# Kernel tuning notes

Measured on AMD Instinct MI355X. Metric: run time of the kernel, lower is better.

## Reference

```python
import jax, jax.numpy as jnp
import numpy as np

TAU = 0.6      # init_tau (membrane decay, also scales surrogate h_t)
TAU_O = 0.6    # init_tau_o (output / eligibility kappa filter)
THR = 0.6      # init_thresh (spike threshold)
LR = 0.05      # e-prop grad accumulation factor


def setup_inputs() -> dict:
    key = jax.random.key(0)
    k0, k1, k2, k3, k4 = jax.random.split(key, 5)
    B, T, NI, NH, NO = 64, 100, 700, 512, 20
    # binary spike inputs / one-hot-ish labels (rand -> threshold keeps SNN semantics)
    x = (jax.random.uniform(k0, (B, T, NI)) < 0.3).astype(jnp.float32)
    label = (jax.random.uniform(k1, (B, T, NO)) < 0.5).astype(jnp.float32)
    # kaiming_normal_ then *0.5 for fc1/out; kaiming_normal_ for recurrent
    w_fc1 = jax.random.normal(k2, (NH, NI), jnp.float32) * (0.5 * np.sqrt(2.0 / NI))
    w_rec = jax.random.normal(k3, (NH, NH), jnp.float32) * np.sqrt(2.0 / NH)
    w_out = jax.random.normal(k4, (NO, NH), jnp.float32) * (0.5 * np.sqrt(2.0 / NH))
    return dict(x=x, label=label, training=1, w_fc1=w_fc1, w_rec=w_rec, w_out=w_out)


def reference(x, label, training, w_fc1, w_rec, w_out):
    B, T, NI = x.shape
    NH = w_fc1.shape[0]
    NO = w_out.shape[0]
    dt = x.dtype

    def step(carry, xs):
        (hm, hs, om, os, tin, trec, tout, ein, erec, prev_hs, gf, gr, go) = carry
        xt, lt = xs  # [B,NI], [B,NO]
        # LIF hidden: decay (with reset-by-spike) + input + recurrent
        hidden_input = xt @ w_fc1.T + hs @ w_rec
        hm = TAU * hm * (1.0 - hs) + hidden_input
        hs = (hm >= THR).astype(dt)
        # LIF output
        om = TAU * om * (1.0 - os) + hs @ w_out.T
        os = (om >= THR).astype(dt)
        err = os - lt
        # surrogate derivative (triangle)
        h_t = TAU * jnp.maximum(0.0, 1.0 - jnp.abs((hm - THR) / THR))
        # presynaptic traces (trace_rec uses z_{t-1})
        tin = TAU * tin + xt
        trec = TAU * trec + prev_hs
        # eligibility traces: per-sample outer products, kappa-filtered
        ein = TAU_O * ein + h_t[:, :, None] * tin[:, None, :]    # [B,NH,NI]
        erec = TAU_O * erec + h_t[:, :, None] * trec[:, None, :]  # [B,NH,NH]
        tout = TAU_O * tout + hs
        # learning signal broadcast from output error
        L = err @ w_out  # [B,NH]
        gf = gf + LR * jnp.einsum('br,bri->ri', L, ein)
        gr = gr + LR * jnp.einsum('br,brj->rj', L, erec)
        go = go + LR * jnp.einsum('bo,br->or', err, tout)
        return (hm, hs, om, os, tin, trec, tout, ein, erec, hs, gf, gr, go), os

    z = lambda *s: jnp.zeros(s, dt)
    carry0 = (z(B, NH), z(B, NH), z(B, NO), z(B, NO), z(B, NI), z(B, NH),
              z(B, NH), z(B, NH, NI), z(B, NH, NH), z(B, NH),
              z(NH, NI), z(NH, NH), z(NO, NH))
    xs = (jnp.swapaxes(x, 0, 1), jnp.swapaxes(label, 0, 1))  # time-major
    carryF, outs = jax.lax.scan(step, carry0, xs)
    outputs = jnp.swapaxes(outs, 0, 1)  # [B,T,NO]
    return outputs, carryF[10], carryF[11], carryF[12]
```

## Files before the change

kernel.cpp:

```cpp
#include <hip/hip_runtime.h>
#include <hip/hip_bf16.h>

constexpr int kB  = 64;
constexpr int kT  = 100;
constexpr int kNI = 700;
constexpr int kNH = 512;
constexpr int kNO = 20;
constexpr float TAU   = 0.6f;
constexpr float TAU_O = 0.6f;
constexpr float THR   = 0.6f;
constexpr float LR    = 0.05f;

constexpr size_t BNH = (size_t)kB * kNH;
constexpr size_t BNI = (size_t)kB * kNI;
constexpr size_t BNO = (size_t)kB * kNO;
constexpr int kK   = kT * kB;
constexpr int kKP  = 704;

typedef __attribute__((ext_vector_type(8))) short short8;
typedef __attribute__((ext_vector_type(4))) float f32x4;

constexpr size_t O_XW   = 0;
constexpr size_t O_PGF  = 0;
constexpr size_t O_PGR  = 1572864;
constexpr size_t O_PGO  = 2621440;
constexpr size_t O_HSUR = 3276800;
constexpr size_t O_ERR  = 6553600;
constexpr size_t O_MTB  = 6681600;
constexpr size_t O_TRB  = 8320000;
constexpr size_t O_MSK  = 9958400;
constexpr size_t O_TIB  = 10060800;
constexpr size_t WS_FLOATS = 12300800;

constexpr size_t OUT_GF = (size_t)kB * kT * kNO;
constexpr size_t OUT_GR = OUT_GF + (size_t)kNH * kNI;
constexpr size_t OUT_GO = OUT_GR + (size_t)kNH * kNH;

__global__ __launch_bounds__(256) void k_xw2(const float* __restrict__ x,
                                             const float* __restrict__ wfc,
                                             float* __restrict__ XW) {
    int bx = blockIdx.x;
    int mt = bx % 50, nt = bx / 50;
    int m0 = mt * 128, n0 = nt * 128;
    int tid = threadIdx.x, tx = tid & 15, ty = tid >> 4;
    __shared__ float As[128][20];
    __shared__ float Bs[16][128];
    float acc[8][8] = {};
    int arow = tid >> 1, ahalf = tid & 1;
    int bb = (m0 + arow) & 63, tt = (m0 + arow) >> 6;
    const float* ap = x + ((size_t)bb * kT + tt) * kNI;
    const float* wp = wfc + (size_t)(n0 + arow) * kNI;
    for (int k0 = 0; k0 < kKP; k0 += 16) {
        #pragma unroll
        for (int u = 0; u < 2; u++) {
            int k = k0 + ahalf * 8 + u * 4;
            float4 v = (k + 3 < kNI) ? *(const float4*)(ap + k)
                                     : make_float4(0.f, 0.f, 0.f, 0.f);
            *(float4*)&As[arow][ahalf * 8 + u * 4] = v;
        }
        {
            int kb = k0 + ahalf * 8;
            float4 v0 = (kb + 3 < kNI) ? *(const float4*)(wp + kb)
                                       : make_float4(0.f, 0.f, 0.f, 0.f);
            float4 v1 = (kb + 7 < kNI) ? *(const float4*)(wp + kb + 4)
                                       : make_float4(0.f, 0.f, 0.f, 0.f);
            int c = ahalf * 8;
            Bs[c + 0][arow] = v0.x; Bs[c + 1][arow] = v0.y;
            Bs[c + 2][arow] = v0.z; Bs[c + 3][arow] = v0.w;
            Bs[c + 4][arow] = v1.x; Bs[c + 5][arow] = v1.y;
            Bs[c + 6][arow] = v1.z; Bs[c + 7][arow] = v1.w;
        }
        __syncthreads();
        #pragma unroll
        for (int kk = 0; kk < 16; kk++) {
            float av[8];
            #pragma unroll
            for (int i = 0; i < 4; i++) {
                av[i]     = As[ty * 4 + i][kk];
                av[4 + i] = As[64 + ty * 4 + i][kk];
            }
            float4 b0 = *(const float4*)&Bs[kk][tx * 4];
            float4 b1 = *(const float4*)&Bs[kk][64 + tx * 4];
            float bvv[8] = {b0.x, b0.y, b0.z, b0.w, b1.x, b1.y, b1.z, b1.w};
            #pragma unroll
            for (int i = 0; i < 8; i++)
                #pragma unroll
                for (int j = 0; j < 8; j++) acc[i][j] += av[i] * bvv[j];
        }
        __syncthreads();
    }
    #pragma unroll
    for (int i = 0; i < 8; i++) {
        int m = m0 + ((i < 4) ? (ty * 4 + i) : (64 + ty * 4 + i - 4));
        float* dst = XW + (size_t)m * kNH + n0;
        *(float4*)(dst + tx * 4)      = make_float4(acc[i][0], acc[i][1], acc[i][2], acc[i][3]);
        *(float4*)(dst + 64 + tx * 4) = make_float4(acc[i][4], acc[i][5], acc[i][6], acc[i][7]);
    }
}

__global__ __launch_bounds__(832) void k_forward(float* __restrict__ ws,
                                                 const float* __restrict__ label,
                                                 const float* __restrict__ w_rec,
                                                 const float* __restrict__ w_out,
                                                 float* __restrict__ dout,
                                                 unsigned long long* __restrict__ gmask,
                                                 const float* __restrict__ x) {
    __shared__ float wout_ld[kNO * kNH];
    __shared__ float partial[8][kNH];
    __shared__ unsigned long long mh[kT * 8];
    __shared__ float errh[kT * kNO];

    int bxg = blockIdx.x, tid = threadIdx.x;
    if (bxg >= kB) {
        int idx = (bxg - kB) * 832 + tid;
        if (idx < (int)BNI) {
            int b = idx / kNI, i = idx - b * kNI;
            const float* xp = x + (size_t)b * kT * kNI + i;
            unsigned short* tib = (unsigned short*)(ws + O_TIB);
            size_t rowoff = (size_t)i * kK + (size_t)b * 100;
            float v = 0.f;
            for (int tq = 0; tq < 25; tq++) {
                unsigned long long w8 = 0;
                #pragma unroll
                for (int u = 0; u < 4; u++) {
                    int t = tq * 4 + u;
                    v = TAU * v + xp[(size_t)t * kNI];
                    __hip_bfloat16 bv = __float2bfloat16(v);
                    w8 |= ((unsigned long long)*(unsigned short*)&bv) << (16 * u);
                }
                *(unsigned long long*)&tib[rowoff + tq * 4] = w8;
            }
        }
        return;
    }

    int b = bxg;
    int wave = tid >> 6, lane = tid & 63;
    const f32x4* wr4 = (const f32x4*)w_rec;
    for (int e = tid; e < kNO * kNH; e += 832) wout_ld[e] = w_out[e];
    float hm = 0.f, sp_prev = 0.f;
    float om_r[4] = {0.f, 0.f, 0.f, 0.f}, os_r[4] = {0.f, 0.f, 0.f, 0.f};
    int q = wave - 8;
    const int coff = lane * 2;
    __syncthreads();

    for (int t = 0; t < kT; t++) {
        float xw = 0.f;
        if (wave < 8) {
            xw = ws[O_XW + ((size_t)t * 64 + b) * kNH + tid];
            unsigned long long m = (t > 0) ? mh[(t - 1) * 8 + wave] : 0ull;
            const size_t base = (size_t)wave * 64;
            f32x4 s0 = {0.f, 0.f, 0.f, 0.f}, s1 = s0;
            while (m) {
                int j = __builtin_ctzll(m); m &= m - 1;
                const f32x4* r = wr4 + (base + j) * 128 + coff;
                s0 += r[0]; s1 += r[1];
            }
            *(f32x4*)&partial[wave][lane * 8]     = s0;
            *(f32x4*)&partial[wave][lane * 8 + 4] = s1;
        } else if (t > 0) {
            int to = t - 1;
            unsigned long long mk[8];
            #pragma unroll
            for (int k = 0; k < 8; k++) mk[k] = mh[to * 8 + k];
            #pragma unroll
            for (int r = 0; r < 4; r++) {
                int o = q * 4 + r;
                float p = 0.f;
                #pragma unroll
                for (int k = 0; k < 8; k++)
                    if ((mk[k] >> lane) & 1) p += wout_ld[o * kNH + 64 * k + lane];
                #pragma unroll
                for (int off = 32; off >= 1; off >>= 1) p += __shfl_xor(p, off);
                if (lane == 0) {
                    float om_n = TAU * om_r[r] * (1.f - os_r[r]) + p;
                    float os_n = (om_n >= THR) ? 1.f : 0.f;
                    om_r[r] = om_n; os_r[r] = os_n;
                    errh[to * kNO + o] = os_n - label[((size_t)b * kT + to) * kNO + o];
                    dout[((size_t)b * kT + to) * kNO + o] = os_n;
                }
            }
        }
        __syncthreads();
        if (tid < kNH) {
            float rec = ((partial[0][tid] + partial[1][tid]) + (partial[2][tid] + partial[3][tid]))
                      + ((partial[4][tid] + partial[5][tid]) + (partial[6][tid] + partial[7][tid]));
            hm = TAU * hm * (1.f - sp_prev) + (xw + rec);
            bool v = (hm >= THR);
            float sp = v ? 1.f : 0.f;
            sp_prev = sp;
            ws[O_HSUR + (size_t)t * BNH + (size_t)b * kNH + tid] =
                TAU * fmaxf(0.f, 1.f - fabsf(hm - THR) * (1.f / THR));
            unsigned long long bal = __ballot(v);
            if (lane == 0) {
                mh[t * 8 + wave] = bal;
                gmask[((size_t)t * 64 + b) * 8 + wave] = bal;
            }
        }
        __syncthreads();
    }
    if (wave >= 8) {
        int to = kT - 1;
        unsigned long long mk[8];
        #pragma unroll
        for (int k = 0; k < 8; k++) mk[k] = mh[to * 8 + k];
        #pragma unroll
        for (int r = 0; r < 4; r++) {
            int o = q * 4 + r;
            float p = 0.f;
            #pragma unroll
            for (int k = 0; k < 8; k++)
                if ((mk[k] >> lane) & 1) p += wout_ld[o * kNH + 64 * k + lane];
            #pragma unroll
            for (int off = 32; off >= 1; off >>= 1) p += __shfl_xor(p, off);
            if (lane == 0) {
                float om_n = TAU * om_r[r] * (1.f - os_r[r]) + p;
                float os_n = (om_n >= THR) ? 1.f : 0.f;
                errh[to * kNO + o] = os_n - label[((size_t)b * kT + to) * kNO + o];
                dout[((size_t)b * kT + to) * kNO + o] = os_n;
            }
        }
    }
    if (tid < kNH) {
        unsigned short* trb = (unsigned short*)(ws + O_TRB);
        size_t rowoff = (size_t)tid * kK + (size_t)b * 100;
        int w = tid >> 6, bit = tid & 63;
        float v = 0.f, p = 0.f;
        for (int tq = 0; tq < 25; tq++) {
            unsigned long long w8 = 0;
            #pragma unroll
            for (int u = 0; u < 4; u++) {
                int t = tq * 4 + u;
                v = TAU * v + p;
                __hip_bfloat16 bv = __float2bfloat16(v);
                w8 |= ((unsigned long long)*(unsigned short*)&bv) << (16 * u);
                p = (float)((mh[t * 8 + w] >> bit) & 1ull);
            }
            *(unsigned long long*)&trb[rowoff + tq * 4] = w8;
        }
    }
    __syncthreads();
    if (wave == 8 && lane < kNO) {
        float v = 0.f;
        for (int t = kT - 1; t >= 0; t--) {
            v = errh[t * kNO + lane] + TAU_O * v;
            errh[t * kNO + lane] = v;
            ws[O_ERR + (size_t)t * BNO + (size_t)b * kNO + lane] = v;
        }
    }
    __syncthreads();
    if (tid < kNH) {
        float wreg[kNO];
        #pragma unroll
        for (int o = 0; o < kNO; o++) wreg[o] = wout_ld[o * kNH + tid];
        unsigned short* mtb = (unsigned short*)(ws + O_MTB);
        size_t rowoff = (size_t)tid * kK + (size_t)b * 100;
        for (int tq = 0; tq < 25; tq++) {
            unsigned long long w8 = 0;
            #pragma unroll
            for (int u = 0; u < 4; u++) {
                int t = tq * 4 + u;
                float s = 0.f;
                #pragma unroll
                for (int o = 0; o < kNO; o++) s += errh[t * kNO + o] * wreg[o];
                float val = LR * s * ws[O_HSUR + (size_t)t * BNH + (size_t)b * kNH + tid];
                __hip_bfloat16 bv = __float2bfloat16(val);
                w8 |= ((unsigned long long)*(unsigned short*)&bv) << (16 * u);
            }
            *(unsigned long long*)&mtb[rowoff + tq * 4] = w8;
        }
    }
}

__global__ __launch_bounds__(256) void k_grads(float* __restrict__ ws) {
    __shared__ unsigned short As[128 * 72];
    __shared__ unsigned short Bs[128 * 72];
    int bx = blockIdx.x, tid = threadIdx.x;

    if (bx < 160) {
        constexpr int KC = kK / 4, BK = 64, LDT = 72;
        const unsigned short* A = (const unsigned short*)(ws + O_MTB);
        const unsigned short* B;
        float* Cpart;
        int Nrows, ldc, s, mt, nt;
        if (bx < 96) {
            s = bx & 3; mt = (bx >> 2) & 3; nt = bx >> 4;
            B = (const unsigned short*)(ws + O_TIB);
            Cpart = ws + O_PGF; Nrows = kNI; ldc = 768;
        } else {
            int v = bx - 96;
            s = v & 3; mt = (v >> 2) & 3; nt = v >> 4;
            B = (const unsigned short*)(ws + O_TRB);
            Cpart = ws + O_PGR; Nrows = kNH; ldc = kNH;
        }
        int m0 = mt * 128, n0 = nt * 128, k0 = s * KC;
        int wave = tid >> 6, lane = tid & 63;
        int wm = wave & 1, wn = wave >> 1;
        f32x4 acc[4][4];
        #pragma unroll
        for (int i = 0; i < 4; i++)
            #pragma unroll
            for (int j = 0; j < 4; j++) acc[i][j] = (f32x4){0.f, 0.f, 0.f, 0.f};

        for (int kb = 0; kb < KC; kb += BK) {
            int kg = k0 + kb;
            #pragma unroll
            for (int p = 0; p < 4; p++) {
                int f = tid + p * 256;
                int row = f >> 3, seg = f & 7;
                *(short8*)&As[row * LDT + seg * 8] =
                    *(const short8*)&A[(size_t)(m0 + row) * kK + kg + seg * 8];
                short8 bv = {};
                if (n0 + row < Nrows)
                    bv = *(const short8*)&B[(size_t)(n0 + row) * kK + kg + seg * 8];
                *(short8*)&Bs[row * LDT + seg * 8] = bv;
            }
            __syncthreads();
            #pragma unroll
            for (int h = 0; h < 2; h++) {
                int kof = h * 32 + (lane >> 4) * 8;
                short8 af[4], bf[4];
                #pragma unroll
                for (int i = 0; i < 4; i++)
                    af[i] = *(short8*)&As[(wm * 64 + i * 16 + (lane & 15)) * LDT + kof];
                #pragma unroll
                for (int j = 0; j < 4; j++)
                    bf[j] = *(short8*)&Bs[(wn * 64 + j * 16 + (lane & 15)) * LDT + kof];
                #pragma unroll
                for (int i = 0; i < 4; i++)
                    #pragma unroll
                    for (int j = 0; j < 4; j++)
                        acc[i][j] = __builtin_amdgcn_mfma_f32_16x16x32_bf16(af[i], bf[j], acc[i][j], 0, 0, 0);
            }
            __syncthreads();
        }
        float* C = Cpart + (size_t)s * kNH * ldc;
        int rbase = (lane >> 4) * 4, col = lane & 15;
        #pragma unroll
        for (int i = 0; i < 4; i++)
            #pragma unroll
            for (int j = 0; j < 4; j++) {
                int n = n0 + wn * 64 + j * 16 + col;
                #pragma unroll
                for (int r = 0; r < 4; r++) {
                    int m = m0 + wm * 64 + i * 16 + rbase + r;
                    C[(size_t)m * ldc + n] = acc[i][j][r];
                }
            }
    } else {
        float* Asf = (float*)As;
        float* Bsf = (float*)Bs;
        const float* A = ws + O_ERR;
        const unsigned long long* gm = (const unsigned long long*)(ws + O_MSK);
        int v = bx - 160;
        int s = v & 7, nt = v >> 3;
        int n0 = nt * 64, k0 = s * 800;
        int w0 = n0 >> 6;
        int tx = tid & 15, ty = tid >> 4;
        float acc[4][4] = {};
        for (int kb = 0; kb < 800; kb += 16) {
            #pragma unroll
            for (int e = tid; e < 1024; e += 256) {
                int kk = e >> 6, c = e & 63;
                size_t gk = (size_t)(k0 + kb + kk);
                Asf[kk * 64 + c] = (c < kNO) ? A[gk * kNO + c] : 0.f;
                Bsf[kk * 64 + c] = (float)((gm[gk * 8 + w0] >> c) & 1ull);
            }
            __syncthreads();
            #pragma unroll
            for (int kk = 0; kk < 16; kk++) {
                float4 av = *(const float4*)&Asf[kk * 64 + ty * 4];
                float4 bv = *(const float4*)&Bsf[kk * 64 + tx * 4];
                float aa[4] = {av.x, av.y, av.z, av.w};
                float bb[4] = {bv.x, bv.y, bv.z, bv.w};
                #pragma unroll
                for (int a = 0; a < 4; a++)
                    #pragma unroll
                    for (int c = 0; c < 4; c++) acc[a][c] += aa[a] * bb[c];
            }
            __syncthreads();
        }
        float* Cs = ws + O_PGO + (size_t)s * kNO * kNH;
        #pragma unroll
        for (int a = 0; a < 4; a++) {
            int m = ty * 4 + a;
            if (m >= kNO) continue;
            #pragma unroll
            for (int c = 0; c < 4; c++)
                Cs[(size_t)m * kNH + n0 + tx * 4 + c] = acc[a][c];
        }
    }
}

__global__ void k_reduce_all(const float* __restrict__ ws, float* __restrict__ dout) {
    int idx = blockIdx.x * 256 + threadIdx.x;
    const int NGF = kNH * kNI, NGR = kNH * kNH, NGO = kNO * kNH;
    float s = 0.f;
    if (idx < NGF) {
        int m = idx / kNI, n = idx - m * kNI;
        size_t src = O_PGF + (size_t)m * 768 + n;
        #pragma unroll
        for (int k = 0; k < 4; k++) s += ws[src + (size_t)k * kNH * 768];
        dout[OUT_GF + idx] = s;
    } else if (idx < NGF + NGR) {
        int j = idx - NGF;
        #pragma unroll
        for (int k = 0; k < 4; k++) s += ws[O_PGR + j + (size_t)k * NGR];
        dout[OUT_GR + j] = s;
    } else if (idx < NGF + NGR + NGO) {
        int j = idx - NGF - NGR;
        #pragma unroll
        for (int k = 0; k < 8; k++) s += ws[O_PGO + (size_t)k * NGO + j];
        dout[OUT_GO + j] = LR * s;
    }
}

extern "C" void kernel_launch(void* const* d_in, const int* in_sizes, int n_in,
                              void* d_out, int out_size, void* d_ws, size_t ws_size,
                              hipStream_t stream) {
    (void)in_sizes; (void)n_in; (void)out_size;
    const float* x     = (const float*)d_in[0];
    const float* label = (const float*)d_in[1];
    const float* w_fc1 = (const float*)d_in[3];
    const float* w_rec = (const float*)d_in[4];
    const float* w_out = (const float*)d_in[5];
    float* out = (float*)d_out;
    float* ws  = (float*)d_ws;

    if (ws_size < WS_FLOATS * sizeof(float)) return;

    unsigned long long* gmask = (unsigned long long*)(ws + O_MSK);

    k_xw2<<<200, 256, 0, stream>>>(x, w_fc1, ws + O_XW);

    k_forward<<<kB + 54, 832, 0, stream>>>(ws, label, w_rec, w_out, out, gmask, x);

    k_grads<<<224, 256, 0, stream>>>(ws);

    k_reduce_all<<<2464, 256, 0, stream>>>(ws, out);
}
```

Measured before the change: 634.0 us.

## Fuse split-K reduction into grads kernel via atomic last-block counters; halve xw2 tile

Removes the separate k_reduce_all launch. Each split-K tile in k_grads now increments a per-tile atomic counter, and the last-arriving block sums the partial results and writes the final gradient. The input-projection GEMM tile width is halved from 128 to 64 columns, doubling the block count to 400 for better CU occupancy. This adds a memset of the counters and serialized reduction work in the last block of each tile.

```diff
diff --git a/kernel.cpp b/kernel.cpp
--- a/kernel.cpp
+++ b/kernel.cpp
@@ -30,7 +30,8 @@
 constexpr size_t O_TRB  = 8320000;
 constexpr size_t O_MSK  = 9958400;
 constexpr size_t O_TIB  = 10060800;
-constexpr size_t WS_FLOATS = 12300800;
+constexpr size_t O_CNT  = 12300800;
+constexpr size_t WS_FLOATS = 12300864;
 
 constexpr size_t OUT_GF = (size_t)kB * kT * kNO;
 constexpr size_t OUT_GR = OUT_GF + (size_t)kNH * kNI;
@@ -41,15 +42,16 @@
                                              float* __restrict__ XW) {
     int bx = blockIdx.x;
     int mt = bx % 50, nt = bx / 50;
-    int m0 = mt * 128, n0 = nt * 128;
+    int m0 = mt * 128, n0 = nt * 64;
     int tid = threadIdx.x, tx = tid & 15, ty = tid >> 4;
     __shared__ float As[128][20];
-    __shared__ float Bs[16][128];
-    float acc[8][8] = {};
+    __shared__ float Bs[16][64];
+    float acc[8][4] = {};
     int arow = tid >> 1, ahalf = tid & 1;
     int bb = (m0 + arow) & 63, tt = (m0 + arow) >> 6;
     const float* ap = x + ((size_t)bb * kT + tt) * kNI;
-    const float* wp = wfc + (size_t)(n0 + arow) * kNI;
+    int br = tid >> 2, bc4 = tid & 3;
+    const float* wp = wfc + (size_t)(n0 + br) * kNI;
     for (int k0 = 0; k0 < kKP; k0 += 16) {
         #pragma unroll
         for (int u = 0; u < 2; u++) {
@@ -59,16 +61,11 @@
             *(float4*)&As[arow][ahalf * 8 + u * 4] = v;
         }
         {
-            int kb = k0 + ahalf * 8;
-            float4 v0 = (kb + 3 < kNI) ? *(const float4*)(wp + kb)
-                                       : make_float4(0.f, 0.f, 0.f, 0.f);
-            float4 v1 = (kb + 7 < kNI) ? *(const float4*)(wp + kb + 4)
-                                       : make_float4(0.f, 0.f, 0.f, 0.f);
-            int c = ahalf * 8;
-            Bs[c + 0][arow] = v0.x; Bs[c + 1][arow] = v0.y;
-            Bs[c + 2][arow] = v0.z; Bs[c + 3][arow] = v0.w;
-            Bs[c + 4][arow] = v1.x; Bs[c + 5][arow] = v1.y;
-            Bs[c + 6][arow] = v1.z; Bs[c + 7][arow] = v1.w;
+            int k = k0 + bc4 * 4;
+            float4 v = (k + 3 < kNI) ? *(const float4*)(wp + k)
+                                     : make_float4(0.f, 0.f, 0.f, 0.f);
+            Bs[bc4 * 4 + 0][br] = v.x; Bs[bc4 * 4 + 1][br] = v.y;
+            Bs[bc4 * 4 + 2][br] = v.z; Bs[bc4 * 4 + 3][br] = v.w;
         }
         __syncthreads();
         #pragma unroll
@@ -80,12 +77,11 @@
                 av[4 + i] = As[64 + ty * 4 + i][kk];
             }
             float4 b0 = *(const float4*)&Bs[kk][tx * 4];
-            float4 b1 = *(const float4*)&Bs[kk][64 + tx * 4];
-            float bvv[8] = {b0.x, b0.y, b0.z, b0.w, b1.x, b1.y, b1.z, b1.w};
+            float bv[4] = {b0.x, b0.y, b0.z, b0.w};
             #pragma unroll
             for (int i = 0; i < 8; i++)
                 #pragma unroll
-                for (int j = 0; j < 8; j++) acc[i][j] += av[i] * bvv[j];
+                for (int j = 0; j < 4; j++) acc[i][j] += av[i] * bv[j];
         }
         __syncthreads();
     }
@@ -93,8 +89,7 @@
     for (int i = 0; i < 8; i++) {
         int m = m0 + ((i < 4) ? (ty * 4 + i) : (64 + ty * 4 + i - 4));
         float* dst = XW + (size_t)m * kNH + n0;
-        *(float4*)(dst + tx * 4)      = make_float4(acc[i][0], acc[i][1], acc[i][2], acc[i][3]);
-        *(float4*)(dst + 64 + tx * 4) = make_float4(acc[i][4], acc[i][5], acc[i][6], acc[i][7]);
+        *(float4*)(dst + tx * 4) = make_float4(acc[i][0], acc[i][1], acc[i][2], acc[i][3]);
     }
 }
 
@@ -272,26 +267,31 @@
     }
 }
 
-__global__ __launch_bounds__(256) void k_grads(float* __restrict__ ws) {
+__global__ __launch_bounds__(256) void k_grads(float* __restrict__ ws,
+                                               float* __restrict__ dout) {
     __shared__ unsigned short As[128 * 72];
     __shared__ unsigned short Bs[128 * 72];
+    __shared__ int isLast;
     int bx = blockIdx.x, tid = threadIdx.x;
+    int* cnt = (int*)(ws + O_CNT);
 
     if (bx < 160) {
         constexpr int KC = kK / 4, BK = 64, LDT = 72;
         const unsigned short* A = (const unsigned short*)(ws + O_MTB);
         const unsigned short* B;
         float* Cpart;
-        int Nrows, ldc, s, mt, nt;
+        int Nrows, ldc, s, mt, nt, tileid;
         if (bx < 96) {
             s = bx & 3; mt = (bx >> 2) & 3; nt = bx >> 4;
             B = (const unsigned short*)(ws + O_TIB);
             Cpart = ws + O_PGF; Nrows = kNI; ldc = 768;
+            tileid = mt + 4 * nt;
         } else {
             int v = bx - 96;
             s = v & 3; mt = (v >> 2) & 3; nt = v >> 4;
             B = (const unsigned short*)(ws + O_TRB);
             Cpart = ws + O_PGR; Nrows = kNH; ldc = kNH;
+            tileid = 24 + mt + 4 * nt;
         }
         int m0 = mt * 128, n0 = nt * 128, k0 = s * KC;
         int wave = tid >> 6, lane = tid & 63;
@@ -347,6 +347,34 @@
                     C[(size_t)m * ldc + n] = acc[i][j][r];
                 }
             }
+        __syncthreads();
+        if (tid == 0)
+            isLast = (__hip_atomic_fetch_add(&cnt[tileid], 1, __ATOMIC_ACQ_REL,
+                                             __HIP_MEMORY_SCOPE_AGENT) == 3);
+        __syncthreads();
+        if (isLast) {
+            if (bx < 96) {
+                for (int e = tid; e < 128 * 128; e += 256) {
+                    int m = m0 + (e >> 7), n = n0 + (e & 127);
+                    if (n < kNI) {
+                        float sv = 0.f;
+                        size_t src = O_PGF + (size_t)m * 768 + n;
+                        #pragma unroll
+                        for (int k = 0; k < 4; k++) sv += ws[src + (size_t)k * kNH * 768];
+                        dout[OUT_GF + (size_t)m * kNI + n] = sv;
+                    }
+                }
+            } else {
+                for (int e = tid; e < 128 * 128; e += 256) {
+                    int m = m0 + (e >> 7), n = n0 + (e & 127);
+                    float sv = 0.f;
+                    size_t src = O_PGR + (size_t)m * kNH + n;
+                    #pragma unroll
+                    for (int k = 0; k < 4; k++) sv += ws[src + (size_t)k * kNH * kNH];
+                    dout[OUT_GR + (size_t)m * kNH + n] = sv;
+                }
+            }
+        }
     } else {
         float* Asf = (float*)As;
         float* Bsf = (float*)Bs;
@@ -384,34 +412,27 @@
         #pragma unroll
         for (int a = 0; a < 4; a++) {
             int m = ty * 4 + a;
-            if (m >= kNO) continue;
-            #pragma unroll
-            for (int c = 0; c < 4; c++)
-                Cs[(size_t)m * kNH + n0 + tx * 4 + c] = acc[a][c];
-        }
-    }
-}
-
-__global__ void k_reduce_all(const float* __restrict__ ws, float* __restrict__ dout) {
-    int idx = blockIdx.x * 256 + threadIdx.x;
-    const int NGF = kNH * kNI, NGR = kNH * kNH, NGO = kNO * kNH;
-    float s = 0.f;
-    if (idx < NGF) {
-        int m = idx / kNI, n = idx - m * kNI;
-        size_t src = O_PGF + (size_t)m * 768 + n;
-        #pragma unroll
-        for (int k = 0; k < 4; k++) s += ws[src + (size_t)k * kNH * 768];
-        dout[OUT_GF + idx] = s;
-    } else if (idx < NGF + NGR) {
-        int j = idx - NGF;
-        #pragma unroll
-        for (int k = 0; k < 4; k++) s += ws[O_PGR + j + (size_t)k * NGR];
-        dout[OUT_GR + j] = s;
-    } else if (idx < NGF + NGR + NGO) {
-        int j = idx - NGF - NGR;
-        #pragma unroll
-        for (int k = 0; k < 8; k++) s += ws[O_PGO + (size_t)k * NGO + j];
-        dout[OUT_GO + j] = LR * s;
+            if (m < kNO) {
+                #pragma unroll
+                for (int c = 0; c < 4; c++)
+                    Cs[(size_t)m * kNH + n0 + tx * 4 + c] = acc[a][c];
+            }
+        }
+        __syncthreads();
+        if (tid == 0)
+            isLast = (__hip_atomic_fetch_add(&cnt[40 + nt], 1, __ATOMIC_ACQ_REL,
+                                             __HIP_MEMORY_SCOPE_AGENT) == 7);
+        __syncthreads();
+        if (isLast) {
+            for (int e = tid; e < kNO * 64; e += 256) {
+                int o = e >> 6, c = e & 63;
+                float sv = 0.f;
+                size_t src = O_PGO + (size_t)o * kNH + n0 + c;
+                #pragma unroll
+                for (int k = 0; k < 8; k++) sv += ws[src + (size_t)k * kNO * kNH];
+                dout[OUT_GO + (size_t)o * kNH + n0 + c] = LR * sv;
+            }
+        }
     }
 }
 
@@ -431,11 +452,12 @@
 
     unsigned long long* gmask = (unsigned long long*)(ws + O_MSK);
 
-    k_xw2<<<200, 256, 0, stream>>>(x, w_fc1, ws + O_XW);
+    hipMemsetAsync(ws + O_CNT, 0, 64 * sizeof(int), stream);
+
+    k_xw2<<<400, 256, 0, stream>>>(x, w_fc1, ws + O_XW);
 
     k_forward<<<kB + 54, 832, 0, stream>>>(ws, label, w_rec, w_out, out, gmask, x);
 
-    k_grads<<<224, 256, 0, stream>>>(ws);
-
-    k_reduce_all<<<2464, 256, 0, stream>>>(ws, out);
+    k_grads<<<224, 256, 0, stream>>>(ws, out);
+
 }
```

New measurement: 608.7 us. -4.0%, faster.
